# Kernel optimization log

Hardware: AMD Instinct MI355X
Metric: run time of the kernel (lower is better)

Reference implementation:

```python
import jax, jax.numpy as jnp
import numpy as np

N_NODES = 100000
N_EDGES = 1600000
N_GRAPHS = 4096
IN_DIM, HID, OUT_DIM = 128, 128, 64
BN_EPS = 1e-5


def gcn_conv(x, W, b, src, dst):
    """PyG GCNConv: symmetric norm with self-loops. x:[N,Fin] -> [N,Fout]."""
    h = x @ W  # [N, Fout]
    ones = jnp.ones((src.shape[0],), dtype=h.dtype)
    deg = jax.ops.segment_sum(ones, dst, num_segments=N_NODES) + 1.0  # +1 for self-loop
    dinv = jax.lax.rsqrt(deg)  # deg >= 1, safe
    norm = dinv[src] * dinv[dst]  # [E]
    msg = h[src] * norm[:, None]  # [E, Fout] gather + scale
    agg = jax.ops.segment_sum(msg, dst, num_segments=N_NODES)
    agg = agg + h * (dinv * dinv)[:, None]  # self-loop term, norm = dinv_i^2
    return agg + b


def batchnorm(x, gamma, beta):
    mu = jnp.mean(x, axis=0)
    var = jnp.mean(jnp.square(x - mu), axis=0)  # biased var, torch BN training mode
    return (x - mu) * jax.lax.rsqrt(var + BN_EPS) * gamma + beta


def setup_inputs() -> dict:
    key = jax.random.key(0)
    ks = jax.random.split(key, 12)
    x = jax.random.normal(ks[0], (N_NODES, IN_DIM), dtype=jnp.float32)
    edge_index = jax.random.randint(ks[1], (2, N_EDGES), 0, N_NODES, dtype=jnp.int64)
    batch = jnp.sort(jax.random.randint(ks[2], (N_NODES,), 0, N_GRAPHS, dtype=jnp.int64))
    def lin(k, fi, fo):
        s = 1.0 / np.sqrt(fi)
        return jax.random.uniform(k, (fi, fo), jnp.float32, -s, s)
    return {
        "x": x, "edge_index": edge_index, "batch": batch,
        "W1": lin(ks[3], IN_DIM, HID), "b1": jnp.zeros((HID,), jnp.float32),
        "g1": jnp.ones((HID,), jnp.float32), "be1": jnp.zeros((HID,), jnp.float32),
        "W2": lin(ks[4], HID, HID), "b2": jnp.zeros((HID,), jnp.float32),
        "g2": jnp.ones((HID,), jnp.float32), "be2": jnp.zeros((HID,), jnp.float32),
        "W3": lin(ks[5], HID, HID), "b3": jnp.zeros((HID,), jnp.float32),
        "g3": jnp.ones((HID,), jnp.float32), "be3": jnp.zeros((HID,), jnp.float32),
        "fcW": lin(ks[6], HID, OUT_DIM),
        "fcb": jax.random.uniform(ks[7], (OUT_DIM,), jnp.float32, -1/np.sqrt(HID), 1/np.sqrt(HID)),
    }


def reference(x, edge_index, batch, W1, b1, g1, be1, W2, b2, g2, be2, W3, b3, g3, be3, fcW, fcb):
    src, dst = edge_index[0], edge_index[1]
    h = jax.nn.relu(batchnorm(gcn_conv(x, W1, b1, src, dst), g1, be1))
    h = jax.nn.relu(batchnorm(gcn_conv(h, W2, b2, src, dst), g2, be2))
    h = jax.nn.relu(batchnorm(gcn_conv(h, W3, b3, src, dst), g3, be3))
    # global mean pool over graphs
    sums = jax.ops.segment_sum(h, batch, num_segments=N_GRAPHS)  # [G, HID]
    cnt = jax.ops.segment_sum(jnp.ones((N_NODES,), h.dtype), batch, num_segments=N_GRAPHS)
    pooled = sums / jnp.maximum(cnt, 1.0)[:, None]
    return pooled @ fcW + fcb
```

## Files before the change

kernel.cpp:

```cpp
#include <hip/hip_runtime.h>

#define NN 100000
#define NE 1600000
#define NG 4096
#define HID 128
#define ODIM 64
#define BN_EPS 1e-5f
#define NBUK 782
#define BPAD 896
#define NZROW 256
#define CHUNK 16384
#define PREP_HIST 256
#define PREP_GOFF 17
#define PREP_W 192

typedef unsigned int u32;
typedef unsigned short u16;
typedef short short8 __attribute__((ext_vector_type(8)));
typedef float f32x4 __attribute__((ext_vector_type(4)));

__device__ inline u32 pack_bf16(float a, float b) {
  u32 ua = __float_as_uint(a), ub = __float_as_uint(b);
  ua += 0x7fffu + ((ua >> 16) & 1u);
  ub += 0x7fffu + ((ub >> 16) & 1u);
  return (ua >> 16) | (ub & 0xffff0000u);
}
__device__ inline u16 bf16_of(float v) {
  u32 ua = __float_as_uint(v);
  ua += 0x7fffu + ((ua >> 16) & 1u);
  return (u16)(ua >> 16);
}
__device__ inline float bf_lo(u32 u) { return __uint_as_float(u << 16); }
__device__ inline float bf_hi(u32 u) { return __uint_as_float(u & 0xffff0000u); }

__global__ __launch_bounds__(256) void k_prep(const int* __restrict__ ei, int* __restrict__ bcnt,
                                              const int* __restrict__ batch, int* __restrict__ goff,
                                              const float* __restrict__ W1, const float* __restrict__ W2,
                                              const float* __restrict__ W3, u16* __restrict__ Wt1,
                                              u16* __restrict__ Wt2, u16* __restrict__ Wt3) {
  __shared__ int h[NBUK];
  int b = blockIdx.x, t = threadIdx.x;
  if (b < PREP_HIST) {
    for (int i = t; i < NBUK; i += 256) h[i] = 0;
    __syncthreads();
    const int stride = PREP_HIST * 256;
    for (int e = b * 256 + t; e < NE; e += stride)
      atomicAdd(&h[ei[NE + e] >> 7], 1);
    __syncthreads();
    for (int i = t; i < NBUK; i += 256)
      if (h[i]) atomicAdd(&bcnt[i], h[i]);
  } else if (b < PREP_HIST + PREP_GOFF) {
    int g = (b - PREP_HIST) * 256 + t;
    if (g <= NG) {
      int lo = 0, hi = NN;
      while (lo < hi) { int mid = (lo + hi) >> 1; if (batch[mid] < g) lo = mid + 1; else hi = mid; }
      goff[g] = lo;
    }
  } else {
    int idx = (b - PREP_HIST - PREP_GOFF) * 256 + t;
    int mat = idx >> 14;
    int rem = idx & 16383;
    int n = rem >> 7, k = rem & 127;
    const float* W = (mat == 0) ? W1 : (mat == 1) ? W2 : W3;
    u16* Wt = (mat == 0) ? Wt1 : (mat == 1) ? Wt2 : Wt3;
    Wt[(n << 7) + k] = bf16_of(W[(k << 7) + n]);
  }
}

__global__ __launch_bounds__(1024) void k_bscan(const int* __restrict__ bcnt, int* __restrict__ bboff,
                                                int* __restrict__ bcur) {
  __shared__ int ls[1024];
  int t = threadIdx.x;
  ls[t] = (t < NBUK) ? bcnt[t] : 0;
  __syncthreads();
  for (int d = 1; d < 1024; d <<= 1) {
    int v = 0;
    if (t >= d) v = ls[t - d];
    __syncthreads();
    ls[t] += v;
    __syncthreads();
  }
  if (t < NBUK) {
    int ex = (t == 0) ? 0 : ls[t - 1];
    bboff[t] = ex;
    bcur[t] = ex;
  }
  if (t == 0) bboff[NBUK] = NE;
}

__global__ __launch_bounds__(1024) void k_bscatter(const int* __restrict__ ei, int* __restrict__ bcur,
                                                   u32* __restrict__ ebuf) {
  __shared__ int cnt[NBUK], rnk[NBUK], base[NBUK];
  int t = threadIdx.x;
  int e0 = blockIdx.x * CHUNK;
  for (int i = t; i < NBUK; i += 1024) { cnt[i] = 0; rnk[i] = 0; }
  __syncthreads();
  for (int i = t; i < CHUNK; i += 1024) {
    int e = e0 + i;
    if (e < NE) atomicAdd(&cnt[ei[NE + e] >> 7], 1);
  }
  __syncthreads();
  for (int i = t; i < NBUK; i += 1024) {
    int c = cnt[i];
    base[i] = c ? atomicAdd(&bcur[i], c) : 0;
  }
  __syncthreads();
  for (int i = t; i < CHUNK; i += 1024) {
    int e = e0 + i;
    if (e < NE) {
      int s = ei[e], d = ei[NE + e];
      int b = d >> 7;
      int r = atomicAdd(&rnk[b], 1);
      ebuf[base[b] + r] = ((u32)(d & 127) << 17) | (u32)s;
    }
  }
}

__global__ __launch_bounds__(256) void k_csr(const u32* __restrict__ ebuf, const int* __restrict__ bboff,
                                             int* __restrict__ off, int* __restrict__ oend,
                                             float* __restrict__ dinv, u32* __restrict__ csrc) {
  __shared__ int cnt[128], scn[128], cur[128];
  int b = blockIdx.x, t = threadIdx.x;
  int n0 = b << 7;
  int ebeg = bboff[b], eend = bboff[b + 1];
  int pboff = ebeg + BPAD * b;
  if (t < 128) cnt[t] = 0;
  __syncthreads();
  for (int e = ebeg + t; e < eend; e += 256) atomicAdd(&cnt[ebuf[e] >> 17], 1);
  __syncthreads();
  int pc = 0;
  if (t < 128) { pc = (cnt[t] + 7) & ~7; scn[t] = pc; }
  __syncthreads();
  for (int d = 1; d < 128; d <<= 1) {
    int v = 0;
    if (t >= d && t < 128) v = scn[t - d];
    __syncthreads();
    if (t < 128) scn[t] += v;
    __syncthreads();
  }
  int nvalid = min(128, NN - n0);
  if (t < 128) {
    int ex = scn[t] - pc;
    cur[t] = ex;
    if (t < nvalid) {
      off[n0 + t] = pboff + ex;
      oend[n0 + t] = pboff + scn[t];
      dinv[n0 + t] = rsqrtf((float)cnt[t] + 1.0f);
    }
  }
  __syncthreads();
  for (int e = ebeg + t; e < eend; e += 256) {
    u32 p = ebuf[e];
    int d = p >> 17;
    int pos = pboff + atomicAdd(&cur[d], 1);
    csrc[pos] = p & 0x1ffffu;
  }
  if (t < 128) {
    int ex = scn[t] - pc;
    for (int i = cnt[t]; i < pc; ++i)
      csrc[pboff + ex + i] = (u32)(NN + ((n0 + t + i) & (NZROW - 1)));
  }
}

__global__ __launch_bounds__(256) void k_gemm1(const float* __restrict__ A, const u16* __restrict__ Wt,
                                               const float* __restrict__ dinv, u16* __restrict__ H) {
  __shared__ u16 Ct[128][128];
  u16 (*At)[32] = (u16 (*)[32])(&Ct[0][0]);
  u16 (*Bt)[32] = (u16 (*)[32])(&Ct[32][0]);

  int t = threadIdx.x;
  int w = t >> 6, l = t & 63;
  int quad = l >> 4, lid = l & 15;
  int row0 = blockIdx.x * 128;

  f32x4 acc[2][8];
#pragma unroll
  for (int mt = 0; mt < 2; ++mt)
#pragma unroll
    for (int nt = 0; nt < 8; ++nt) acc[mt][nt] = (f32x4){0.f, 0.f, 0.f, 0.f};

  int ar = t >> 1;
  int ac = (t & 1) << 4;
  int grow = row0 + ar;
  bool aok = grow < NN;

  for (int k0 = 0; k0 < HID; k0 += 32) {
    float4 f0 = {0, 0, 0, 0}, f1 = {0, 0, 0, 0}, f2 = {0, 0, 0, 0}, f3 = {0, 0, 0, 0};
    if (aok) {
      const float4* ap = (const float4*)(A + (size_t)grow * HID + k0 + ac);
      f0 = ap[0]; f1 = ap[1]; f2 = ap[2]; f3 = ap[3];
    }
    uint4 q0, q1;
    q0.x = pack_bf16(f0.x, f0.y); q0.y = pack_bf16(f0.z, f0.w);
    q0.z = pack_bf16(f1.x, f1.y); q0.w = pack_bf16(f1.z, f1.w);
    q1.x = pack_bf16(f2.x, f2.y); q1.y = pack_bf16(f2.z, f2.w);
    q1.z = pack_bf16(f3.x, f3.y); q1.w = pack_bf16(f3.z, f3.w);
    *(uint4*)&At[ar][ac] = q0;
    *(uint4*)&At[ar][ac + 8] = q1;
    const u16* wp = Wt + (size_t)(t >> 1) * HID + k0 + ac;
    *(uint4*)&Bt[t >> 1][ac]     = ((const uint4*)wp)[0];
    *(uint4*)&Bt[t >> 1][ac + 8] = ((const uint4*)wp)[1];
    __syncthreads();
    short8 a0 = *(const short8*)&At[(w << 5) + lid][quad << 3];
    short8 a1 = *(const short8*)&At[(w << 5) + 16 + lid][quad << 3];
#pragma unroll
    for (int nt = 0; nt < 8; ++nt) {
      short8 b = *(const short8*)&Bt[(nt << 4) + lid][quad << 3];
      acc[0][nt] = __builtin_amdgcn_mfma_f32_16x16x32_bf16(a0, b, acc[0][nt], 0, 0, 0);
      acc[1][nt] = __builtin_amdgcn_mfma_f32_16x16x32_bf16(a1, b, acc[1][nt], 0, 0, 0);
    }
    __syncthreads();
  }

  int valid = min(128, NN - row0);
#pragma unroll
  for (int mt = 0; mt < 2; ++mt) {
#pragma unroll
    for (int r = 0; r < 4; ++r) {
      int rl = (w << 5) + (mt << 4) + (quad << 2) + r;
      float dv = (rl < valid) ? dinv[row0 + rl] : 0.f;
#pragma unroll
      for (int nt = 0; nt < 8; ++nt) {
        Ct[rl][(nt << 4) + lid] = bf16_of(acc[mt][nt][r] * dv);
      }
    }
  }
  __syncthreads();
  u16* Hb = H + (size_t)row0 * HID;
  int tot = valid << 4;
  for (int idx = t; idx < tot; idx += 256) {
    ((uint4*)Hb)[idx] = ((const uint4*)Ct)[idx];
  }
}

__device__ inline u32 bn_pair(u32 v, float2 sc, float2 sh) {
  float a = fmaxf(fmaf(bf_lo(v), sc.x, sh.x), 0.f);
  float b = fmaxf(fmaf(bf_hi(v), sc.y, sh.y), 0.f);
  return pack_bf16(a, b);
}

__global__ __launch_bounds__(256) void k_gemm_b(const u16* __restrict__ A, const u16* __restrict__ Wt,
                                                const float* __restrict__ sums, const float* __restrict__ g,
                                                const float* __restrict__ be,
                                                const float* __restrict__ dinv, u16* __restrict__ H) {
  __shared__ u16 Ct[128][128];
  u16 (*At)[32] = (u16 (*)[32])(&Ct[0][0]);
  u16 (*Bt)[32] = (u16 (*)[32])(&Ct[32][0]);
  float* scsh = (float*)&Ct[64][0];

  int t = threadIdx.x;
  int w = t >> 6, l = t & 63;
  int quad = l >> 4, lid = l & 15;
  int row0 = blockIdx.x * 128;

  if (t < 128) {
    const float invN = 1.0f / (float)NN;
    float mu = sums[t] * invN;
    float var = sums[HID + t] * invN - mu * mu;
    float sc = g[t] * rsqrtf(var + BN_EPS);
    scsh[t] = sc;
    scsh[128 + t] = be[t] - mu * sc;
  }

  f32x4 acc[2][8];
#pragma unroll
  for (int mt = 0; mt < 2; ++mt)
#pragma unroll
    for (int nt = 0; nt < 8; ++nt) acc[mt][nt] = (f32x4){0.f, 0.f, 0.f, 0.f};

  int ar = t >> 1;
  int ac = (t & 1) << 4;
  int grow = row0 + ar;
  bool aok = grow < NN;
  __syncthreads();

  for (int k0 = 0; k0 < HID; k0 += 32) {
    uint4 q0 = {0, 0, 0, 0}, q1 = {0, 0, 0, 0};
    if (aok) {
      const uint4* ap = (const uint4*)(A + (size_t)grow * HID + k0 + ac);
      q0 = ap[0]; q1 = ap[1];
    }
    const float2* scp = (const float2*)(scsh + k0 + ac);
    const float2* shp = (const float2*)(scsh + 128 + k0 + ac);
    q0.x = bn_pair(q0.x, scp[0], shp[0]); q0.y = bn_pair(q0.y, scp[1], shp[1]);
    q0.z = bn_pair(q0.z, scp[2], shp[2]); q0.w = bn_pair(q0.w, scp[3], shp[3]);
    q1.x = bn_pair(q1.x, scp[4], shp[4]); q1.y = bn_pair(q1.y, scp[5], shp[5]);
    q1.z = bn_pair(q1.z, scp[6], shp[6]); q1.w = bn_pair(q1.w, scp[7], shp[7]);
    *(uint4*)&At[ar][ac] = q0;
    *(uint4*)&At[ar][ac + 8] = q1;
    const u16* wp = Wt + (size_t)(t >> 1) * HID + k0 + ac;
    *(uint4*)&Bt[t >> 1][ac]     = ((const uint4*)wp)[0];
    *(uint4*)&Bt[t >> 1][ac + 8] = ((const uint4*)wp)[1];
    __syncthreads();
    short8 a0 = *(const short8*)&At[(w << 5) + lid][quad << 3];
    short8 a1 = *(const short8*)&At[(w << 5) + 16 + lid][quad << 3];
#pragma unroll
    for (int nt = 0; nt < 8; ++nt) {
      short8 b = *(const short8*)&Bt[(nt << 4) + lid][quad << 3];
      acc[0][nt] = __builtin_amdgcn_mfma_f32_16x16x32_bf16(a0, b, acc[0][nt], 0, 0, 0);
      acc[1][nt] = __builtin_amdgcn_mfma_f32_16x16x32_bf16(a1, b, acc[1][nt], 0, 0, 0);
    }
    __syncthreads();
  }

  int valid = min(128, NN - row0);
#pragma unroll
  for (int mt = 0; mt < 2; ++mt) {
#pragma unroll
    for (int r = 0; r < 4; ++r) {
      int rl = (w << 5) + (mt << 4) + (quad << 2) + r;
      float dv = (rl < valid) ? dinv[row0 + rl] : 0.f;
#pragma unroll
      for (int nt = 0; nt < 8; ++nt) {
        Ct[rl][(nt << 4) + lid] = bf16_of(acc[mt][nt][r] * dv);
      }
    }
  }
  __syncthreads();
  u16* Hb = H + (size_t)row0 * HID;
  int tot = valid << 4;
  for (int idx = t; idx < tot; idx += 256) {
    ((uint4*)Hb)[idx] = ((const uint4*)Ct)[idx];
  }
}

__global__ __launch_bounds__(256) void k_agg(const u16* __restrict__ h2, const int* __restrict__ off,
                                             const int* __restrict__ oend, const u32* __restrict__ csrc,
                                             const float* __restrict__ dinv, u16* __restrict__ aggb) {
  int node = (int)((blockIdx.x * 256 + threadIdx.x) >> 6);
  int lane = threadIdx.x & 63;
  if (node >= NN) return;
  int beg = off[node], end = oend[node];
  u32 us = ((const u32*)(h2 + (size_t)node * HID))[lane];
  float ax = bf_lo(us), ay = bf_hi(us);
  for (int e = beg; e < end; e += 8) {
    u32 s[8], v[8];
#pragma unroll
    for (int i = 0; i < 8; ++i) s[i] = csrc[e + i];
#pragma unroll
    for (int i = 0; i < 8; ++i) v[i] = ((const u32*)(h2 + (size_t)s[i] * HID))[lane];
#pragma unroll
    for (int i = 0; i < 8; ++i) { ax += bf_lo(v[i]); ay += bf_hi(v[i]); }
  }
  float di = dinv[node];
  ((u32*)(aggb + (size_t)node * HID))[lane] = pack_bf16(ax * di, ay * di);
}

__global__ __launch_bounds__(256) void k_bnstats(const u16* __restrict__ X, float* __restrict__ buf) {
  __shared__ float lsx[256], lssx[256], lsy[256], lssy[256];
  int t = threadIdx.x;
  int colp = t & 63, grp = t >> 6;
  int rbeg = blockIdx.x * 256, rend = min(rbeg + 256, NN);
  float sx = 0.f, ssx = 0.f, sy = 0.f, ssy = 0.f;
  for (int r = rbeg + grp; r < rend; r += 4) {
    u32 v = ((const u32*)(X + (size_t)r * HID))[colp];
    float a = bf_lo(v), b = bf_hi(v);
    sx += a; ssx = fmaf(a, a, ssx);
    sy += b; ssy = fmaf(b, b, ssy);
  }
  lsx[t] = sx; lssx[t] = ssx; lsy[t] = sy; lssy[t] = ssy;
  __syncthreads();
  if (t < 64) {
    sx = lsx[t] + lsx[t + 64] + lsx[t + 128] + lsx[t + 192];
    ssx = lssx[t] + lssx[t + 64] + lssx[t + 128] + lssx[t + 192];
    sy = lsy[t] + lsy[t + 64] + lsy[t + 128] + lsy[t + 192];
    ssy = lssy[t] + lssy[t + 64] + lssy[t + 128] + lssy[t + 192];
    atomicAdd(&buf[2 * colp], sx);
    atomicAdd(&buf[2 * colp + 1], sy);
    atomicAdd(&buf[HID + 2 * colp], ssx);
    atomicAdd(&buf[HID + 2 * colp + 1], ssy);
  }
}

__global__ __launch_bounds__(256) void k_poolfc(const u16* __restrict__ aggb, const float* __restrict__ sums,
                                                const float* __restrict__ g3, const float* __restrict__ be3,
                                                const int* __restrict__ goff, const float* __restrict__ fcW,
                                                const float* __restrict__ fcb, float* __restrict__ out) {
  __shared__ float ls[4][128];
  int t = threadIdx.x;
  int w = t >> 6, lane = t & 63;
  int gr = blockIdx.x * 4 + w;
  const float invN = 1.0f / (float)NN;
  int f0 = lane << 1, f1 = f0 + 1;
  float mu0 = sums[f0] * invN, mu1 = sums[f1] * invN;
  float v0 = sums[HID + f0] * invN - mu0 * mu0;
  float v1 = sums[HID + f1] * invN - mu1 * mu1;
  float sc0 = g3[f0] * rsqrtf(v0 + BN_EPS), sc1 = g3[f1] * rsqrtf(v1 + BN_EPS);
  float sh0 = be3[f0] - mu0 * sc0, sh1 = be3[f1] - mu1 * sc1;
  int beg = goff[gr], end = goff[gr + 1];
  float ax = 0.f, ay = 0.f;
  for (int r = beg; r < end; ++r) {
    u32 v = ((const u32*)(aggb + (size_t)r * HID))[lane];
    ax += fmaxf(fmaf(bf_lo(v), sc0, sh0), 0.f);
    ay += fmaxf(fmaf(bf_hi(v), sc1, sh1), 0.f);
  }
  float inv = 1.0f / fmaxf((float)(end - beg), 1.0f);
  ls[w][f0] = ax * inv;
  ls[w][f1] = ay * inv;
  __syncthreads();
  float acc = fcb[lane];
#pragma unroll 8
  for (int k = 0; k < HID; ++k) acc = fmaf(ls[w][k], fcW[(size_t)k * ODIM + lane], acc);
  out[(size_t)gr * ODIM + lane] = acc;
}

extern "C" void kernel_launch(void* const* d_in, const int* in_sizes, int n_in,
                              void* d_out, int out_size, void* d_ws, size_t ws_size,
                              hipStream_t stream) {
  const float* x     = (const float*)d_in[0];
  const int*   ei    = (const int*)d_in[1];
  const int*   batch = (const int*)d_in[2];
  const float* W1    = (const float*)d_in[3];
  const float* g1    = (const float*)d_in[5];
  const float* be1   = (const float*)d_in[6];
  const float* W2    = (const float*)d_in[7];
  const float* g2    = (const float*)d_in[9];
  const float* be2   = (const float*)d_in[10];
  const float* W3    = (const float*)d_in[11];
  const float* g3    = (const float*)d_in[13];
  const float* be3   = (const float*)d_in[14];
  const float* fcW   = (const float*)d_in[15];
  const float* fcb   = (const float*)d_in[16];
  float* out = (float*)d_out;

  char* p = (char*)d_ws;
  auto alloc = [&](size_t bytes) { char* r = p; p += (bytes + 255) & ~(size_t)255; return r; };
  int*   bcnt   = (int*)alloc((size_t)NBUK * 4);
  float* bnb    = (float*)alloc(3 * 256 * 4);
  size_t zbytes = (size_t)(p - (char*)d_ws);
  int*   bboff  = (int*)alloc((size_t)(NBUK + 1) * 4);
  int*   bcur   = (int*)alloc((size_t)NBUK * 4);
  int*   off    = (int*)alloc((size_t)NN * 4);
  int*   oend   = (int*)alloc((size_t)NN * 4);
  float* dinv   = (float*)alloc((size_t)NN * 4);
  u32*   ebuf   = (u32*)alloc((size_t)NE * 4);
  u32*   csrc   = (u32*)alloc(((size_t)NE + (size_t)BPAD * NBUK) * 4);
  int*   goff   = (int*)alloc((size_t)(NG + 1) * 4);
  u16*   Wt1    = (u16*)alloc((size_t)HID * HID * 2);
  u16*   Wt2    = (u16*)alloc((size_t)HID * HID * 2);
  u16*   Wt3    = (u16*)alloc((size_t)HID * HID * 2);
  u16*   h2     = (u16*)alloc((size_t)(NN + NZROW) * HID * 2);
  u16*   aggb   = (u16*)alloc((size_t)NN * HID * 2);

  hipMemsetAsync(d_ws, 0, zbytes, stream);
  hipMemsetAsync(h2 + (size_t)NN * HID, 0, (size_t)NZROW * HID * 2, stream);

  const int NB = (NN + 255) / 256;
  const int GB = (NN + 127) / 128;
  const int AGB = NN / 4;
  const int SB = (NE + CHUNK - 1) / CHUNK;

  k_prep<<<PREP_HIST + PREP_GOFF + PREP_W, 256, 0, stream>>>(ei, bcnt, batch, goff, W1, W2, W3, Wt1, Wt2, Wt3);
  k_bscan<<<1, 1024, 0, stream>>>(bcnt, bboff, bcur);
  k_bscatter<<<SB, 1024, 0, stream>>>(ei, bcur, ebuf);
  k_csr<<<NBUK, 256, 0, stream>>>(ebuf, bboff, off, oend, dinv, csrc);

  k_gemm1<<<GB, 256, 0, stream>>>(x, Wt1, dinv, h2);
  k_agg<<<AGB, 256, 0, stream>>>(h2, off, oend, csrc, dinv, aggb);
  k_bnstats<<<NB, 256, 0, stream>>>(aggb, bnb);
  k_gemm_b<<<GB, 256, 0, stream>>>(aggb, Wt2, bnb, g1, be1, dinv, h2);
  k_agg<<<AGB, 256, 0, stream>>>(h2, off, oend, csrc, dinv, aggb);
  k_bnstats<<<NB, 256, 0, stream>>>(aggb, bnb + 256);
  k_gemm_b<<<GB, 256, 0, stream>>>(aggb, Wt3, bnb + 256, g2, be2, dinv, h2);
  k_agg<<<AGB, 256, 0, stream>>>(h2, off, oend, csrc, dinv, aggb);
  k_bnstats<<<NB, 256, 0, stream>>>(aggb, bnb + 512);
  k_poolfc<<<NG / 4, 256, 0, stream>>>(aggb, bnb + 512, g3, be3, goff, fcW, fcb, out);
}
```

Baseline: 525.1 us.

## Compute per-node degrees early and co-launch first GEMM with edge bucket scatter

The edge pass in k_prep now computes per-node in-degree with global atomics instead of per-bucket histograms. A new small kernel derives dinv and the bucket counts from those degrees. Because dinv is then ready before the CSR build, the first GEMM is merged into one launch with the bucket scatter (GEMM blocks and scatter blocks share the grid), so the two independent workloads overlap. k_csr reads degrees directly and skips its counting pass. The cost is global atomics spread over 100k addresses and an extra small launch, and the scatter now runs with 256 threads per block instead of 1024.

```diff
diff --git a/kernel.cpp b/kernel.cpp
--- a/kernel.cpp
+++ b/kernel.cpp
@@ -10,7 +10,9 @@
 #define BPAD 896
 #define NZROW 256
 #define CHUNK 16384
-#define PREP_HIST 256
+#define GB 782
+#define SB 98
+#define PREP_DEG 256
 #define PREP_GOFF 17
 #define PREP_W 192
 
@@ -33,31 +35,25 @@
 __device__ inline float bf_lo(u32 u) { return __uint_as_float(u << 16); }
 __device__ inline float bf_hi(u32 u) { return __uint_as_float(u & 0xffff0000u); }
 
-__global__ __launch_bounds__(256) void k_prep(const int* __restrict__ ei, int* __restrict__ bcnt,
+__global__ __launch_bounds__(256) void k_prep(const int* __restrict__ ei, int* __restrict__ deg,
                                               const int* __restrict__ batch, int* __restrict__ goff,
                                               const float* __restrict__ W1, const float* __restrict__ W2,
                                               const float* __restrict__ W3, u16* __restrict__ Wt1,
                                               u16* __restrict__ Wt2, u16* __restrict__ Wt3) {
-  __shared__ int h[NBUK];
   int b = blockIdx.x, t = threadIdx.x;
-  if (b < PREP_HIST) {
-    for (int i = t; i < NBUK; i += 256) h[i] = 0;
-    __syncthreads();
-    const int stride = PREP_HIST * 256;
+  if (b < PREP_DEG) {
+    const int stride = PREP_DEG * 256;
     for (int e = b * 256 + t; e < NE; e += stride)
-      atomicAdd(&h[ei[NE + e] >> 7], 1);
-    __syncthreads();
-    for (int i = t; i < NBUK; i += 256)
-      if (h[i]) atomicAdd(&bcnt[i], h[i]);
-  } else if (b < PREP_HIST + PREP_GOFF) {
-    int g = (b - PREP_HIST) * 256 + t;
+      atomicAdd(&deg[ei[NE + e]], 1);
+  } else if (b < PREP_DEG + PREP_GOFF) {
+    int g = (b - PREP_DEG) * 256 + t;
     if (g <= NG) {
       int lo = 0, hi = NN;
       while (lo < hi) { int mid = (lo + hi) >> 1; if (batch[mid] < g) lo = mid + 1; else hi = mid; }
       goff[g] = lo;
     }
   } else {
-    int idx = (b - PREP_HIST - PREP_GOFF) * 256 + t;
+    int idx = (b - PREP_DEG - PREP_GOFF) * 256 + t;
     int mat = idx >> 14;
     int rem = idx & 16383;
     int n = rem >> 7, k = rem & 127;
@@ -67,6 +63,23 @@
   }
 }
 
+__global__ __launch_bounds__(256) void k_nodeprep(const int* __restrict__ deg, float* __restrict__ dinv,
+                                                  int* __restrict__ bcnt) {
+  __shared__ int s[256];
+  int b = blockIdx.x, t = threadIdx.x;
+  int i = b * 256 + t;
+  int d = (i < NN) ? deg[i] : 0;
+  if (i < NN) dinv[i] = rsqrtf((float)d + 1.0f);
+  s[t] = d;
+  __syncthreads();
+  for (int dd = 64; dd > 0; dd >>= 1) {
+    if ((t & 127) < dd) s[t] += s[t + dd];
+    __syncthreads();
+  }
+  if (t == 0) bcnt[2 * b] = s[0];
+  if (t == 128) bcnt[2 * b + 1] = s[128];
+}
+
 __global__ __launch_bounds__(1024) void k_bscan(const int* __restrict__ bcnt, int* __restrict__ bboff,
                                                 int* __restrict__ bcur) {
   __shared__ int ls[1024];
@@ -88,45 +101,116 @@
   if (t == 0) bboff[NBUK] = NE;
 }
 
-__global__ __launch_bounds__(1024) void k_bscatter(const int* __restrict__ ei, int* __restrict__ bcur,
-                                                   u32* __restrict__ ebuf) {
-  __shared__ int cnt[NBUK], rnk[NBUK], base[NBUK];
+__global__ __launch_bounds__(256) void k_gb1(const float* __restrict__ A, const u16* __restrict__ Wt,
+                                             const float* __restrict__ dinv, u16* __restrict__ H,
+                                             const int* __restrict__ ei, int* __restrict__ bcur,
+                                             u32* __restrict__ ebuf) {
+  __shared__ u16 Ct[128][128];
   int t = threadIdx.x;
-  int e0 = blockIdx.x * CHUNK;
-  for (int i = t; i < NBUK; i += 1024) { cnt[i] = 0; rnk[i] = 0; }
-  __syncthreads();
-  for (int i = t; i < CHUNK; i += 1024) {
-    int e = e0 + i;
-    if (e < NE) atomicAdd(&cnt[ei[NE + e] >> 7], 1);
-  }
-  __syncthreads();
-  for (int i = t; i < NBUK; i += 1024) {
-    int c = cnt[i];
-    base[i] = c ? atomicAdd(&bcur[i], c) : 0;
-  }
-  __syncthreads();
-  for (int i = t; i < CHUNK; i += 1024) {
-    int e = e0 + i;
-    if (e < NE) {
-      int s = ei[e], d = ei[NE + e];
-      int b = d >> 7;
-      int r = atomicAdd(&rnk[b], 1);
-      ebuf[base[b] + r] = ((u32)(d & 127) << 17) | (u32)s;
+  if (blockIdx.x < GB) {
+    u16 (*At)[32] = (u16 (*)[32])(&Ct[0][0]);
+    u16 (*Bt)[32] = (u16 (*)[32])(&Ct[32][0]);
+    int w = t >> 6, l = t & 63;
+    int quad = l >> 4, lid = l & 15;
+    int row0 = blockIdx.x * 128;
+
+    f32x4 acc[2][8];
+#pragma unroll
+    for (int mt = 0; mt < 2; ++mt)
+#pragma unroll
+      for (int nt = 0; nt < 8; ++nt) acc[mt][nt] = (f32x4){0.f, 0.f, 0.f, 0.f};
+
+    int ar = t >> 1;
+    int ac = (t & 1) << 4;
+    int grow = row0 + ar;
+    bool aok = grow < NN;
+
+    for (int k0 = 0; k0 < HID; k0 += 32) {
+      float4 f0 = {0, 0, 0, 0}, f1 = {0, 0, 0, 0}, f2 = {0, 0, 0, 0}, f3 = {0, 0, 0, 0};
+      if (aok) {
+        const float4* ap = (const float4*)(A + (size_t)grow * HID + k0 + ac);
+        f0 = ap[0]; f1 = ap[1]; f2 = ap[2]; f3 = ap[3];
+      }
+      uint4 q0, q1;
+      q0.x = pack_bf16(f0.x, f0.y); q0.y = pack_bf16(f0.z, f0.w);
+      q0.z = pack_bf16(f1.x, f1.y); q0.w = pack_bf16(f1.z, f1.w);
+      q1.x = pack_bf16(f2.x, f2.y); q1.y = pack_bf16(f2.z, f2.w);
+      q1.z = pack_bf16(f3.x, f3.y); q1.w = pack_bf16(f3.z, f3.w);
+      *(uint4*)&At[ar][ac] = q0;
+      *(uint4*)&At[ar][ac + 8] = q1;
+      const u16* wp = Wt + (size_t)(t >> 1) * HID + k0 + ac;
+      *(uint4*)&Bt[t >> 1][ac]     = ((const uint4*)wp)[0];
+      *(uint4*)&Bt[t >> 1][ac + 8] = ((const uint4*)wp)[1];
+      __syncthreads();
+      short8 a0 = *(const short8*)&At[(w << 5) + lid][quad << 3];
+      short8 a1 = *(const short8*)&At[(w << 5) + 16 + lid][quad << 3];
+#pragma unroll
+      for (int nt = 0; nt < 8; ++nt) {
+        short8 b = *(const short8*)&Bt[(nt << 4) + lid][quad << 3];
+        acc[0][nt] = __builtin_amdgcn_mfma_f32_16x16x32_bf16(a0, b, acc[0][nt], 0, 0, 0);
+        acc[1][nt] = __builtin_amdgcn_mfma_f32_16x16x32_bf16(a1, b, acc[1][nt], 0, 0, 0);
+      }
+      __syncthreads();
+    }
+
+    int valid = min(128, NN - row0);
+#pragma unroll
+    for (int mt = 0; mt < 2; ++mt) {
+#pragma unroll
+      for (int r = 0; r < 4; ++r) {
+        int rl = (w << 5) + (mt << 4) + (quad << 2) + r;
+        float dv = (rl < valid) ? dinv[row0 + rl] : 0.f;
+#pragma unroll
+        for (int nt = 0; nt < 8; ++nt) {
+          Ct[rl][(nt << 4) + lid] = bf16_of(acc[mt][nt][r] * dv);
+        }
+      }
+    }
+    __syncthreads();
+    u16* Hb = H + (size_t)row0 * HID;
+    int tot = valid << 4;
+    for (int idx = t; idx < tot; idx += 256) {
+      ((uint4*)Hb)[idx] = ((const uint4*)Ct)[idx];
+    }
+  } else {
+    int* cnt  = (int*)&Ct[0][0];
+    int* rnk  = cnt + NBUK;
+    int* base = rnk + NBUK;
+    int e0 = (blockIdx.x - GB) * CHUNK;
+    for (int i = t; i < NBUK; i += 256) { cnt[i] = 0; rnk[i] = 0; }
+    __syncthreads();
+    for (int i = t; i < CHUNK; i += 256) {
+      int e = e0 + i;
+      if (e < NE) atomicAdd(&cnt[ei[NE + e] >> 7], 1);
+    }
+    __syncthreads();
+    for (int i = t; i < NBUK; i += 256) {
+      int c = cnt[i];
+      base[i] = c ? atomicAdd(&bcur[i], c) : 0;
+    }
+    __syncthreads();
+    for (int i = t; i < CHUNK; i += 256) {
+      int e = e0 + i;
+      if (e < NE) {
+        int s = ei[e], d = ei[NE + e];
+        int b = d >> 7;
+        int r = atomicAdd(&rnk[b], 1);
+        ebuf[base[b] + r] = ((u32)(d & 127) << 17) | (u32)s;
+      }
     }
   }
 }
 
 __global__ __launch_bounds__(256) void k_csr(const u32* __restrict__ ebuf, const int* __restrict__ bboff,
-                                             int* __restrict__ off, int* __restrict__ oend,
-                                             float* __restrict__ dinv, u32* __restrict__ csrc) {
+                                             const int* __restrict__ deg, int* __restrict__ off,
+                                             int* __restrict__ oend, u32* __restrict__ csrc) {
   __shared__ int cnt[128], scn[128], cur[128];
   int b = blockIdx.x, t = threadIdx.x;
   int n0 = b << 7;
   int ebeg = bboff[b], eend = bboff[b + 1];
   int pboff = ebeg + BPAD * b;
-  if (t < 128) cnt[t] = 0;
-  __syncthreads();
-  for (int e = ebeg + t; e < eend; e += 256) atomicAdd(&cnt[ebuf[e] >> 17], 1);
+  int nvalid = min(128, NN - n0);
+  if (t < 128) cnt[t] = (t < nvalid) ? deg[n0 + t] : 0;
   __syncthreads();
   int pc = 0;
   if (t < 128) { pc = (cnt[t] + 7) & ~7; scn[t] = pc; }
@@ -138,14 +222,12 @@
     if (t < 128) scn[t] += v;
     __syncthreads();
   }
-  int nvalid = min(128, NN - n0);
   if (t < 128) {
     int ex = scn[t] - pc;
     cur[t] = ex;
     if (t < nvalid) {
       off[n0 + t] = pboff + ex;
       oend[n0 + t] = pboff + scn[t];
-      dinv[n0 + t] = rsqrtf((float)cnt[t] + 1.0f);
     }
   }
   __syncthreads();
@@ -159,77 +241,6 @@
     int ex = scn[t] - pc;
     for (int i = cnt[t]; i < pc; ++i)
       csrc[pboff + ex + i] = (u32)(NN + ((n0 + t + i) & (NZROW - 1)));
-  }
-}
-
-__global__ __launch_bounds__(256) void k_gemm1(const float* __restrict__ A, const u16* __restrict__ Wt,
-                                               const float* __restrict__ dinv, u16* __restrict__ H) {
-  __shared__ u16 Ct[128][128];
-  u16 (*At)[32] = (u16 (*)[32])(&Ct[0][0]);
-  u16 (*Bt)[32] = (u16 (*)[32])(&Ct[32][0]);
-
-  int t = threadIdx.x;
-  int w = t >> 6, l = t & 63;
-  int quad = l >> 4, lid = l & 15;
-  int row0 = blockIdx.x * 128;
-
-  f32x4 acc[2][8];
-#pragma unroll
-  for (int mt = 0; mt < 2; ++mt)
-#pragma unroll
-    for (int nt = 0; nt < 8; ++nt) acc[mt][nt] = (f32x4){0.f, 0.f, 0.f, 0.f};
-
-  int ar = t >> 1;
-  int ac = (t & 1) << 4;
-  int grow = row0 + ar;
-  bool aok = grow < NN;
-
-  for (int k0 = 0; k0 < HID; k0 += 32) {
-    float4 f0 = {0, 0, 0, 0}, f1 = {0, 0, 0, 0}, f2 = {0, 0, 0, 0}, f3 = {0, 0, 0, 0};
-    if (aok) {
-      const float4* ap = (const float4*)(A + (size_t)grow * HID + k0 + ac);
-      f0 = ap[0]; f1 = ap[1]; f2 = ap[2]; f3 = ap[3];
-    }
-    uint4 q0, q1;
-    q0.x = pack_bf16(f0.x, f0.y); q0.y = pack_bf16(f0.z, f0.w);
-    q0.z = pack_bf16(f1.x, f1.y); q0.w = pack_bf16(f1.z, f1.w);
-    q1.x = pack_bf16(f2.x, f2.y); q1.y = pack_bf16(f2.z, f2.w);
-    q1.z = pack_bf16(f3.x, f3.y); q1.w = pack_bf16(f3.z, f3.w);
-    *(uint4*)&At[ar][ac] = q0;
-    *(uint4*)&At[ar][ac + 8] = q1;
-    const u16* wp = Wt + (size_t)(t >> 1) * HID + k0 + ac;
-    *(uint4*)&Bt[t >> 1][ac]     = ((const uint4*)wp)[0];
-    *(uint4*)&Bt[t >> 1][ac + 8] = ((const uint4*)wp)[1];
-    __syncthreads();
-    short8 a0 = *(const short8*)&At[(w << 5) + lid][quad << 3];
-    short8 a1 = *(const short8*)&At[(w << 5) + 16 + lid][quad << 3];
-#pragma unroll
-    for (int nt = 0; nt < 8; ++nt) {
-      short8 b = *(const short8*)&Bt[(nt << 4) + lid][quad << 3];
-      acc[0][nt] = __builtin_amdgcn_mfma_f32_16x16x32_bf16(a0, b, acc[0][nt], 0, 0, 0);
-      acc[1][nt] = __builtin_amdgcn_mfma_f32_16x16x32_bf16(a1, b, acc[1][nt], 0, 0, 0);
-    }
-    __syncthreads();
-  }
-
-  int valid = min(128, NN - row0);
-#pragma unroll
-  for (int mt = 0; mt < 2; ++mt) {
-#pragma unroll
-    for (int r = 0; r < 4; ++r) {
-      int rl = (w << 5) + (mt << 4) + (quad << 2) + r;
-      float dv = (rl < valid) ? dinv[row0 + rl] : 0.f;
-#pragma unroll
-      for (int nt = 0; nt < 8; ++nt) {
-        Ct[rl][(nt << 4) + lid] = bf16_of(acc[mt][nt][r] * dv);
-      }
-    }
-  }
-  __syncthreads();
-  u16* Hb = H + (size_t)row0 * HID;
-  int tot = valid << 4;
-  for (int idx = t; idx < tot; idx += 256) {
-    ((uint4*)Hb)[idx] = ((const uint4*)Ct)[idx];
   }
 }
 
@@ -425,9 +436,10 @@
 
   char* p = (char*)d_ws;
   auto alloc = [&](size_t bytes) { char* r = p; p += (bytes + 255) & ~(size_t)255; return r; };
-  int*   bcnt   = (int*)alloc((size_t)NBUK * 4);
+  int*   deg    = (int*)alloc((size_t)NN * 4);
   float* bnb    = (float*)alloc(3 * 256 * 4);
   size_t zbytes = (size_t)(p - (char*)d_ws);
+  int*   bcnt   = (int*)alloc((size_t)NBUK * 4);
   int*   bboff  = (int*)alloc((size_t)(NBUK + 1) * 4);
   int*   bcur   = (int*)alloc((size_t)NBUK * 4);
   int*   off    = (int*)alloc((size_t)NN * 4);
@@ -446,16 +458,14 @@
   hipMemsetAsync(h2 + (size_t)NN * HID, 0, (size_t)NZROW * HID * 2, stream);
 
   const int NB = (NN + 255) / 256;
-  const int GB = (NN + 127) / 128;
   const int AGB = NN / 4;
-  const int SB = (NE + CHUNK - 1) / CHUNK;
-
-  k_prep<<<PREP_HIST + PREP_GOFF + PREP_W, 256, 0, stream>>>(ei, bcnt, batch, goff, W1, W2, W3, Wt1, Wt2, Wt3);
+
+  k_prep<<<PREP_DEG + PREP_GOFF + PREP_W, 256, 0, stream>>>(ei, deg, batch, goff, W1, W2, W3, Wt1, Wt2, Wt3);
+  k_nodeprep<<<NB, 256, 0, stream>>>(deg, dinv, bcnt);
   k_bscan<<<1, 1024, 0, stream>>>(bcnt, bboff, bcur);
-  k_bscatter<<<SB, 1024, 0, stream>>>(ei, bcur, ebuf);
-  k_csr<<<NBUK, 256, 0, stream>>>(ebuf, bboff, off, oend, dinv, csrc);
-
-  k_gemm1<<<GB, 256, 0, stream>>>(x, Wt1, dinv, h2);
+  k_gb1<<<GB + SB, 256, 0, stream>>>(x, Wt1, dinv, h2, ei, bcur, ebuf);
+  k_csr<<<NBUK, 256, 0, stream>>>(ebuf, bboff, deg, off, oend, csrc);
+
   k_agg<<<AGB, 256, 0, stream>>>(h2, off, oend, csrc, dinv, aggb);
   k_bnstats<<<NB, 256, 0, stream>>>(aggb, bnb);
   k_gemm_b<<<GB, 256, 0, stream>>>(aggb, Wt2, bnb, g1, be1, dinv, h2);
```

New measurement: 635.8 us. 1.21x slower.
